# Optimization experiments

Measured on AMD Instinct MI355X. Metric: run time of the kernel, lower is better.

## Reference

```python
import jax, jax.numpy as jnp
import numpy as np

T, D, M1, M2, K = 8192, 512, 2048, 2048, 1024


def setup_inputs() -> dict:
    key = jax.random.key(0)
    k = jax.random.split(key, 6)
    s1 = 1.0 / np.sqrt(D + M1)   # layer 1 init scale (1/sqrt(M1_in + M2_out))
    s2 = 1.0 / np.sqrt(M1 + M2)  # layer 2 init scale
    return {
        "X": jax.random.normal(k[0], (T, D), jnp.float32),
        # RNN layer 1 (D -> M1)
        "Wx1": jax.random.normal(k[1], (D, M1), jnp.float32) * s1,
        "Wh1": jax.random.normal(k[2], (M1, M1), jnp.float32) * s1,
        "bh1": jnp.zeros((M1,), jnp.float32),
        "h01": jnp.zeros((M1,), jnp.float32),
        # RNN layer 2 (M1 -> M2)
        "Wx2": jax.random.normal(k[3], (M1, M2), jnp.float32) * s2,
        "Wh2": jax.random.normal(k[4], (M2, M2), jnp.float32) * s2,
        "bh2": jnp.zeros((M2,), jnp.float32),
        "h02": jnp.zeros((M2,), jnp.float32),
        # logistic = nn.Linear(M2, K); store weight as (M2, K) so y = h @ Wl + bl
        "Wl": jax.random.normal(k[5], (M2, K), jnp.float32) / np.sqrt(M2),
        "bl": jnp.zeros((K,), jnp.float32),
    }


def rnn_layer(X, Wx, Wh, bh, h0):
    # X: (T, Din) -> out: (T, Dout). hidden_t = relu((X@Wx)_t + hidden_{t-1} @ Wh + bh)
    Xp = X @ Wx  # (T, Dout) dense GEMM, precomputed as in the torch code

    def step(h, x):
        h = jax.nn.relu(x + h @ Wh + bh)
        return h, h

    _, out = jax.lax.scan(step, h0, Xp)
    return out


def reference(X, Wx1, Wh1, bh1, h01, Wx2, Wh2, bh2, h02, Wl, bl):
    h = rnn_layer(X, Wx1, Wh1, bh1, h01)
    h = rnn_layer(h, Wx2, Wh2, bh2, h02)
    return h @ Wl + bl  # (T, K) logits
```

## Files before the change

kernel.cpp:

```cpp
#include <hip/hip_runtime.h>
#include <cstdint>
#include <cstddef>

#define TT 8192
#define DD 512
#define MM 2048
#define KK 1024

typedef float f32x4 __attribute__((ext_vector_type(4)));
typedef int   i32x4 __attribute__((ext_vector_type(4)));
typedef unsigned int uint32;

__device__ __forceinline__ void coh_load32(const uint32* p, i32x4& a, i32x4& b) {
  asm volatile("global_load_dwordx4 %0, %2, off sc0 sc1\n\t"
               "global_load_dwordx4 %1, %2, off offset:16 sc0 sc1\n\t"
               "s_waitcnt vmcnt(0)"
               : "=v"(a), "=v"(b) : "v"(p) : "memory");
}
__device__ __forceinline__ void coh_store32(uint32* p, i32x4 a, i32x4 b) {
  asm volatile("global_store_dwordx4 %0, %1, off sc0 sc1\n\t"
               "global_store_dwordx4 %0, %2, off offset:16 sc0 sc1"
               :: "v"(p), "v"(a), "v"(b) : "memory");
}

__device__ __forceinline__ float scrub(float v) {
  return __int_as_float(__float_as_int(v) & 0x7fffffff);
}
__device__ __forceinline__ uint32 bf16r(float f) {
  uint32 u = __float_as_uint(f);
  return (u + 0x7fffu + ((u >> 16) & 1u)) >> 16;
}
__device__ __forceinline__ uint32 pack2(float lo, float hi) {
  return bf16r(lo) | (bf16r(hi) << 16);
}
__device__ __forceinline__ float bflo(uint32 u) { return __uint_as_float(u << 16); }
__device__ __forceinline__ float bfhi(uint32 u) { return __uint_as_float(u & 0xffff0000u); }

__global__ void __launch_bounds__(256) gemm_bias_f32(
    const float* __restrict__ A, const float* __restrict__ B,
    const float* __restrict__ bias, float* __restrict__ C,
    int M, int N, int K)
{
  __shared__ float As[16][128];
  __shared__ float Bs[16][128];
  const int tid = threadIdx.x;
  const int tx = tid & 15, ty = tid >> 4;
  const int row0 = blockIdx.y * 128, col0 = blockIdx.x * 128;
  const int arow = tid >> 1;
  const int ak0  = (tid & 1) * 8;
  const int brow = tid >> 4;
  const int bcol = (tid & 15) * 8;

  const float* Aptr = A + (size_t)(row0 + arow) * K + ak0;
  const float* Bptr = B + (size_t)brow * N + col0 + bcol;

  float acc[8][8];
  #pragma unroll
  for (int i = 0; i < 8; ++i)
    #pragma unroll
    for (int j = 0; j < 8; ++j) acc[i][j] = 0.f;

  for (int kk = 0; kk < K; kk += 16) {
    float4 a0 = *(const float4*)(Aptr + kk);
    float4 a1 = *(const float4*)(Aptr + kk + 4);
    float4 b0 = *(const float4*)(Bptr + (size_t)kk * N);
    float4 b1 = *(const float4*)(Bptr + (size_t)kk * N + 4);
    __syncthreads();
    As[ak0+0][arow] = a0.x; As[ak0+1][arow] = a0.y;
    As[ak0+2][arow] = a0.z; As[ak0+3][arow] = a0.w;
    As[ak0+4][arow] = a1.x; As[ak0+5][arow] = a1.y;
    As[ak0+6][arow] = a1.z; As[ak0+7][arow] = a1.w;
    *(float4*)&Bs[brow][bcol]     = b0;
    *(float4*)&Bs[brow][bcol + 4] = b1;
    __syncthreads();
    #pragma unroll
    for (int k = 0; k < 16; ++k) {
      float4 av0 = *(float4*)&As[k][ty*8];
      float4 av1 = *(float4*)&As[k][ty*8 + 4];
      float4 bv0 = *(float4*)&Bs[k][tx*4];
      float4 bv1 = *(float4*)&Bs[k][64 + tx*4];
      float ar[8] = {av0.x,av0.y,av0.z,av0.w,av1.x,av1.y,av1.z,av1.w};
      float br[8] = {bv0.x,bv0.y,bv0.z,bv0.w,bv1.x,bv1.y,bv1.z,bv1.w};
      #pragma unroll
      for (int i = 0; i < 8; ++i)
        #pragma unroll
        for (int j = 0; j < 8; ++j)
          acc[i][j] += ar[i] * br[j];
    }
  }

  float4 bi0 = *(const float4*)&bias[col0 + tx*4];
  float4 bi1 = *(const float4*)&bias[col0 + 64 + tx*4];
  #pragma unroll
  for (int i = 0; i < 8; ++i) {
    size_t r = (size_t)(row0 + ty*8 + i) * N;
    float4 o0 = make_float4(acc[i][0]+bi0.x, acc[i][1]+bi0.y, acc[i][2]+bi0.z, acc[i][3]+bi0.w);
    float4 o1 = make_float4(acc[i][4]+bi1.x, acc[i][5]+bi1.y, acc[i][6]+bi1.z, acc[i][7]+bi1.w);
    *(float4*)&C[r + col0 + tx*4]      = o0;
    *(float4*)&C[r + col0 + 64 + tx*4] = o1;
  }
}

__global__ void __launch_bounds__(256, 1) rnn_fused(
    const float* __restrict__ Xp1, uint32* __restrict__ H1b,
    uint32* __restrict__ H2b, float* __restrict__ H2f,
    const float* __restrict__ Wh1, const float* __restrict__ Wx2,
    const float* __restrict__ Wh2, const float* __restrict__ h01,
    const float* __restrict__ h02, const float* __restrict__ bh2)
{
  __shared__ __align__(16) unsigned char smem[139392];
  const int tid  = threadIdx.x;
  const int lane = tid & 63;
  const int wv   = tid >> 6;

  if (blockIdx.x < 128) {
    const int w = blockIdx.x;
    float*  WL   = (float*)smem;
    uint32* h1p  = (uint32*)(smem + 131072);
    float*  hout = (float*)(smem + 135168);

    for (int r = 0; r < 8; ++r) {
      const int k = tid + 256*r;
      const float* src = &Wh1[(size_t)k*MM + 16*w];
      #pragma unroll
      for (int c4 = 0; c4 < 4; ++c4) {
        float4 q = *(const float4*)(src + 4*c4);
        WL[(4*c4+0)*2048 + k] = q.x;
        WL[(4*c4+1)*2048 + k] = q.y;
        WL[(4*c4+2)*2048 + k] = q.z;
        WL[(4*c4+3)*2048 + k] = q.w;
      }
    }
    const int cbase = 16*w + 4*wv;
    f32x4 xc = {0.f,0.f,0.f,0.f}, xn = xc;
    if (lane == 0) xc = *(const f32x4*)&Xp1[cbase];
    __syncthreads();

    for (int t = 0; t < TT; ++t) {
      if (tid < 128) {
        const int g = tid;
        if (t == 0) {
          uint32 d[8];
          #pragma unroll
          for (int j = 0; j < 8; ++j)
            d[j] = pack2(h01[16*g + 2*j], h01[16*g + 2*j + 1]);
          *(i32x4*)&h1p[8*g]     = *(i32x4*)&d[0];
          *(i32x4*)&h1p[8*g + 4] = *(i32x4*)&d[4];
        } else {
          const uint32* src = H1b + (size_t)(t-1)*1024 + 8*g;
          i32x4 a, b;
          for (;;) {
            coh_load32(src, a, b);
            if ((((a.x|a.y|a.z|a.w|b.x|b.y|b.z|b.w) & 0x80008000u)) == 0) break;
            __builtin_amdgcn_s_sleep(1);
          }
          *(i32x4*)&h1p[8*g]     = a;
          *(i32x4*)&h1p[8*g + 4] = b;
        }
      }
      if (lane == 0 && t + 1 < TT)
        xn = *(const f32x4*)&Xp1[(size_t)(t+1)*MM + cbase];
      __syncthreads();

      float s0=0.f, s1=0.f, s2=0.f, s3=0.f;
      #pragma unroll
      for (int i = 0; i < 8; ++i) {
        const int k0 = 4*lane + 256*i;
        uint2 dw = *(uint2*)&h1p[k0 >> 1];
        f32x4 h = {bflo(dw.x), bfhi(dw.x), bflo(dw.y), bfhi(dw.y)};
        f32x4 q0 = *(f32x4*)&WL[(4*wv+0)*2048 + k0];
        f32x4 q1 = *(f32x4*)&WL[(4*wv+1)*2048 + k0];
        f32x4 q2 = *(f32x4*)&WL[(4*wv+2)*2048 + k0];
        f32x4 q3 = *(f32x4*)&WL[(4*wv+3)*2048 + k0];
        s0 += h.x*q0.x + h.y*q0.y + h.z*q0.z + h.w*q0.w;
        s1 += h.x*q1.x + h.y*q1.y + h.z*q1.z + h.w*q1.w;
        s2 += h.x*q2.x + h.y*q2.y + h.z*q2.z + h.w*q2.w;
        s3 += h.x*q3.x + h.y*q3.y + h.z*q3.z + h.w*q3.w;
      }
      #pragma unroll
      for (int off = 32; off; off >>= 1) {
        s0 += __shfl_xor(s0, off); s1 += __shfl_xor(s1, off);
        s2 += __shfl_xor(s2, off); s3 += __shfl_xor(s3, off);
      }
      if (lane == 0) {
        f32x4 y;
        y.x = scrub(fmaxf(xc.x + s0, 0.f));
        y.y = scrub(fmaxf(xc.y + s1, 0.f));
        y.z = scrub(fmaxf(xc.z + s2, 0.f));
        y.w = scrub(fmaxf(xc.w + s3, 0.f));
        *(f32x4*)&hout[4*wv] = y;
        xc = xn;
      }
      __syncthreads();

      if (tid == 0) {
        uint32 d[8];
        #pragma unroll
        for (int j = 0; j < 8; ++j) d[j] = pack2(hout[2*j], hout[2*j+1]);
        coh_store32(H1b + (size_t)t*1024 + 8*w, *(i32x4*)&d[0], *(i32x4*)&d[4]);
      }
    }
  } else {
    const int w = blockIdx.x - 128;
    unsigned short* W2p = (unsigned short*)smem;
    uint32* h1p  = (uint32*)(smem + 131072);
    uint32* h2p  = (uint32*)(smem + 135168);
    float*  hout = (float*)(smem + 139264);

    for (int r = 0; r < 16; ++r) {
      const int k = tid + 256*r;
      const float* src = (k < MM) ? &Wx2[(size_t)k*MM + 16*w]
                                  : &Wh2[(size_t)(k-MM)*MM + 16*w];
      #pragma unroll
      for (int c4 = 0; c4 < 4; ++c4) {
        float4 q = *(const float4*)(src + 4*c4);
        const int c = 4*c4;
        W2p[((c+0)>>1)*8192 + 2*k + ((c+0)&1)] = (unsigned short)bf16r(q.x);
        W2p[((c+1)>>1)*8192 + 2*k + ((c+1)&1)] = (unsigned short)bf16r(q.y);
        W2p[((c+2)>>1)*8192 + 2*k + ((c+2)&1)] = (unsigned short)bf16r(q.z);
        W2p[((c+3)>>1)*8192 + 2*k + ((c+3)&1)] = (unsigned short)bf16r(q.w);
      }
    }
    const int cbase = 16*w + 4*wv;
    f32x4 bv = {0.f,0.f,0.f,0.f};
    if (lane == 0) bv = *(const f32x4*)&bh2[cbase];
    __syncthreads();

    const int cp0 = 2*wv;

    for (int t = 0; t < TT; ++t) {
      if (tid < 128) {
        const int g = tid;
        const uint32* p1 = H1b + (size_t)t*1024 + 8*g;
        i32x4 a, b;
        for (;;) {
          coh_load32(p1, a, b);
          if ((((a.x|a.y|a.z|a.w|b.x|b.y|b.z|b.w) & 0x80008000u)) == 0) break;
          __builtin_amdgcn_s_sleep(1);
        }
        *(i32x4*)&h1p[8*g]     = a;
        *(i32x4*)&h1p[8*g + 4] = b;
      }
      __syncthreads();

      float s0=0.f, s1=0.f, s2=0.f, s3=0.f;
      #pragma unroll
      for (int i = 0; i < 8; ++i) {
        const int k0 = 4*lane + 256*i;
        uint2 dw = *(uint2*)&h1p[k0 >> 1];
        f32x4 h = {bflo(dw.x), bfhi(dw.x), bflo(dw.y), bfhi(dw.y)};
        uint4 qa = *(uint4*)&W2p[(cp0+0)*8192 + 2*k0];
        uint4 qb = *(uint4*)&W2p[(cp0+1)*8192 + 2*k0];
        s0 += h.x*bflo(qa.x) + h.y*bflo(qa.y) + h.z*bflo(qa.z) + h.w*bflo(qa.w);
        s1 += h.x*bfhi(qa.x) + h.y*bfhi(qa.y) + h.z*bfhi(qa.z) + h.w*bfhi(qa.w);
        s2 += h.x*bflo(qb.x) + h.y*bflo(qb.y) + h.z*bflo(qb.z) + h.w*bflo(qb.w);
        s3 += h.x*bfhi(qb.x) + h.y*bfhi(qb.y) + h.z*bfhi(qb.z) + h.w*bfhi(qb.w);
      }

      if (tid < 128) {
        const int g = tid;
        if (t == 0) {
          uint32 d[8];
          #pragma unroll
          for (int j = 0; j < 8; ++j)
            d[j] = pack2(h02[16*g + 2*j], h02[16*g + 2*j + 1]);
          *(i32x4*)&h2p[8*g]     = *(i32x4*)&d[0];
          *(i32x4*)&h2p[8*g + 4] = *(i32x4*)&d[4];
        } else {
          const uint32* p2 = H2b + (size_t)(t-1)*1024 + 8*g;
          i32x4 c, d;
          for (;;) {
            coh_load32(p2, c, d);
            if ((((c.x|c.y|c.z|c.w|d.x|d.y|d.z|d.w) & 0x80008000u)) == 0) break;
            __builtin_amdgcn_s_sleep(1);
          }
          *(i32x4*)&h2p[8*g]     = c;
          *(i32x4*)&h2p[8*g + 4] = d;
        }
      }
      __syncthreads();

      #pragma unroll
      for (int i = 0; i < 8; ++i) {
        const int k0 = 4*lane + 256*i;
        const int kw = 2048 + k0;
        uint2 dw = *(uint2*)&h2p[k0 >> 1];
        f32x4 h = {bflo(dw.x), bfhi(dw.x), bflo(dw.y), bfhi(dw.y)};
        uint4 qa = *(uint4*)&W2p[(cp0+0)*8192 + 2*kw];
        uint4 qb = *(uint4*)&W2p[(cp0+1)*8192 + 2*kw];
        s0 += h.x*bflo(qa.x) + h.y*bflo(qa.y) + h.z*bflo(qa.z) + h.w*bflo(qa.w);
        s1 += h.x*bfhi(qa.x) + h.y*bfhi(qa.y) + h.z*bfhi(qa.z) + h.w*bfhi(qa.w);
        s2 += h.x*bflo(qb.x) + h.y*bflo(qb.y) + h.z*bflo(qb.z) + h.w*bflo(qb.w);
        s3 += h.x*bfhi(qb.x) + h.y*bfhi(qb.y) + h.z*bfhi(qb.z) + h.w*bfhi(qb.w);
      }
      #pragma unroll
      for (int off = 32; off; off >>= 1) {
        s0 += __shfl_xor(s0, off); s1 += __shfl_xor(s1, off);
        s2 += __shfl_xor(s2, off); s3 += __shfl_xor(s3, off);
      }
      if (lane == 0) {
        f32x4 y;
        y.x = scrub(fmaxf(s0 + bv.x, 0.f));
        y.y = scrub(fmaxf(s1 + bv.y, 0.f));
        y.z = scrub(fmaxf(s2 + bv.z, 0.f));
        y.w = scrub(fmaxf(s3 + bv.w, 0.f));
        *(f32x4*)&H2f[(size_t)t*MM + cbase] = y;
        *(f32x4*)&hout[4*wv] = y;
      }
      __syncthreads();

      if (tid == 0) {
        uint32 d[8];
        #pragma unroll
        for (int j = 0; j < 8; ++j) d[j] = pack2(hout[2*j], hout[2*j+1]);
        coh_store32(H2b + (size_t)t*1024 + 8*w, *(i32x4*)&d[0], *(i32x4*)&d[4]);
      }
    }
  }
}

__device__ __forceinline__ void coh_load2f(const int* p, i32x4& a, i32x4& b) {
  asm volatile("global_load_dwordx4 %0, %2, off sc0 sc1\n\t"
               "global_load_dwordx4 %1, %2, off offset:16 sc0 sc1\n\t"
               "s_waitcnt vmcnt(0)"
               : "=v"(a), "=v"(b) : "v"(p) : "memory");
}
__global__ void __launch_bounds__(256, 1) rnn_scan_f32(
    const float* __restrict__ Xp, float* __restrict__ H,
    const float* __restrict__ Wh, const float* __restrict__ h0)
{
  __shared__ float h_s[MM];
  __shared__ float h_out[8];
  const int tid  = threadIdx.x;
  const int wg   = blockIdx.x;
  const int lane = tid & 63;
  const int wv   = tid >> 6;
  const int c0   = wg * 8 + wv * 2;

  float4 w0[8], w1[8];
  #pragma unroll
  for (int i = 0; i < 8; ++i) {
    const int kb = lane*4 + 256*i;
    float2 e0 = *(const float2*)&Wh[(size_t)(kb+0)*MM + c0];
    float2 e1 = *(const float2*)&Wh[(size_t)(kb+1)*MM + c0];
    float2 e2 = *(const float2*)&Wh[(size_t)(kb+2)*MM + c0];
    float2 e3 = *(const float2*)&Wh[(size_t)(kb+3)*MM + c0];
    w0[i] = make_float4(e0.x, e1.x, e2.x, e3.x);
    w1[i] = make_float4(e0.y, e1.y, e2.y, e3.y);
  }

  for (int t = 0; t < TT; ++t) {
    float4 ha, hb;
    if (t == 0) {
      ha = ((const float4*)h0)[tid*2];
      hb = ((const float4*)h0)[tid*2 + 1];
    } else {
      const int* src = (const int*)(H + (size_t)(t-1)*MM + tid*8);
      i32x4 a, b;
      do { coh_load2f(src, a, b); }
      while ((a.x | a.y | a.z | a.w | b.x | b.y | b.z | b.w) < 0);
      ha = make_float4(__int_as_float(a.x), __int_as_float(a.y),
                       __int_as_float(a.z), __int_as_float(a.w));
      hb = make_float4(__int_as_float(b.x), __int_as_float(b.y),
                       __int_as_float(b.z), __int_as_float(b.w));
    }
    float xv = 0.f;
    if (lane < 2) xv = Xp[(size_t)t*MM + c0 + lane];
    ((float4*)h_s)[tid*2]     = ha;
    ((float4*)h_s)[tid*2 + 1] = hb;
    __syncthreads();

    float s0 = 0.f, s1 = 0.f;
    #pragma unroll
    for (int i = 0; i < 8; ++i) {
      float4 h4 = *(float4*)&h_s[lane*4 + 256*i];
      s0 += h4.x*w0[i].x + h4.y*w0[i].y + h4.z*w0[i].z + h4.w*w0[i].w;
      s1 += h4.x*w1[i].x + h4.y*w1[i].y + h4.z*w1[i].z + h4.w*w1[i].w;
    }
    #pragma unroll
    for (int off = 32; off; off >>= 1) {
      s0 += __shfl_xor(s0, off);
      s1 += __shfl_xor(s1, off);
    }
    if (lane < 2) {
      float s = (lane == 0) ? s0 : s1;
      h_out[wv*2 + lane] = scrub(fmaxf(xv + s, 0.f));
    }
    __syncthreads();
    if (tid == 0) {
      i32x4 o0 = *(i32x4*)&h_out[0];
      i32x4 o1 = *(i32x4*)&h_out[4];
      coh_store32((uint32*)(H + (size_t)t*MM + wg*8), o0, o1);
    }
  }
}

extern "C" void kernel_launch(void* const* d_in, const int* in_sizes, int n_in,
                              void* d_out, int out_size, void* d_ws, size_t ws_size,
                              hipStream_t stream) {
  (void)in_sizes; (void)n_in; (void)out_size;

  const float* X   = (const float*)d_in[0];
  const float* Wx1 = (const float*)d_in[1];
  const float* Wh1 = (const float*)d_in[2];
  const float* bh1 = (const float*)d_in[3];
  const float* h01 = (const float*)d_in[4];
  const float* Wx2 = (const float*)d_in[5];
  const float* Wh2 = (const float*)d_in[6];
  const float* bh2 = (const float*)d_in[7];
  const float* h02 = (const float*)d_in[8];
  const float* Wl  = (const float*)d_in[9];
  const float* bl  = (const float*)d_in[10];
  float* out = (float*)d_out;

  const size_t NBUF = (size_t)TT * MM;
  dim3 blk(256);

  if (ws_size >= 3 * NBUF * sizeof(float)) {
    float*  Xp1 = (float*)d_ws;
    float*  H2f = Xp1 + NBUF;
    uint32* H1b = (uint32*)(H2f + NBUF);
    uint32* H2b = H1b + (size_t)TT * 1024;

    (void)hipMemsetAsync(H1b, 0xFF, 2 * (size_t)TT * 1024 * sizeof(uint32), stream);

    gemm_bias_f32<<<dim3(MM/128, TT/128), blk, 0, stream>>>(X, Wx1, bh1, Xp1, TT, MM, DD);

    {
      const float* xp = Xp1; uint32* h1b = H1b; uint32* h2b = H2b; float* h2f = H2f;
      const float* wh1 = Wh1; const float* wx2 = Wx2; const float* wh2 = Wh2;
      const float* h01p = h01; const float* h02p = h02; const float* bh2p = bh2;
      void* args[] = {&xp, &h1b, &h2b, &h2f, &wh1, &wx2, &wh2, &h01p, &h02p, &bh2p};
      (void)hipLaunchCooperativeKernel((const void*)rnn_fused, dim3(256), blk, args, 0, stream);
    }

    gemm_bias_f32<<<dim3(KK/128, TT/128), blk, 0, stream>>>(H2f, Wl, bl, out, TT, KK, MM);
  } else {
    float* bufA = (float*)d_ws;
    float* bufB = bufA + NBUF;

    (void)hipMemsetAsync(bufB, 0xFF, NBUF * sizeof(float), stream);
    gemm_bias_f32<<<dim3(MM/128, TT/128), blk, 0, stream>>>(X, Wx1, bh1, bufA, TT, MM, DD);
    {
      const float* xp = bufA; float* h = bufB; const float* wh = Wh1; const float* h0p = h01;
      void* args[] = {&xp, &h, &wh, &h0p};
      (void)hipLaunchCooperativeKernel((const void*)rnn_scan_f32, dim3(256), blk, args, 0, stream);
    }
    gemm_bias_f32<<<dim3(MM/128, TT/128), blk, 0, stream>>>(bufB, Wx2, bh2, bufA, TT, MM, MM);
    (void)hipMemsetAsync(bufB, 0xFF, NBUF * sizeof(float), stream);
    {
      const float* xp = bufA; float* h = bufB; const float* wh = Wh2; const float* h0p = h02;
      void* args[] = {&xp, &h, &wh, &h0p};
      (void)hipLaunchCooperativeKernel((const void*)rnn_scan_f32, dim3(256), blk, args, 0, stream);
    }
    gemm_bias_f32<<<dim3(KK/128, TT/128), blk, 0, stream>>>(bufA, Wl, bl, out, TT, KK, MM);
  }
}
```

Before: 24.13 ms.

## Prefetch next H1 and overlap H2 polling with compute in fused RNN

Each wave's lane 0 now writes its packed bf16 outputs straight to the global exchange buffer, which removes a barrier and the single-thread gather/store step per timestep. The layer-2 blocks double-buffer the layer-1 hidden state in LDS. They issue non-blocking loads for the next H1 row and the previous H2 row before the matvec, then wait only afterwards, so global-memory latency overlaps the compute. The layer-1 spin loop drops its sleep. The cost is more complex synchronization and a risk of subtle ordering bugs across blocks.

Result: slower. 29.89 ms (+23.9%).

```diff
diff --git a/kernel.cpp b/kernel.cpp
--- a/kernel.cpp
+++ b/kernel.cpp
@@ -9,6 +9,7 @@
 
 typedef float f32x4 __attribute__((ext_vector_type(4)));
 typedef int   i32x4 __attribute__((ext_vector_type(4)));
+typedef int   i32x2 __attribute__((ext_vector_type(2)));
 typedef unsigned int uint32;
 
 __device__ __forceinline__ void coh_load32(const uint32* p, i32x4& a, i32x4& b) {
@@ -17,12 +18,23 @@
                "s_waitcnt vmcnt(0)"
                : "=v"(a), "=v"(b) : "v"(p) : "memory");
 }
+__device__ __forceinline__ void issue32(const uint32* p, i32x4& a, i32x4& b) {
+  asm volatile("global_load_dwordx4 %0, %2, off sc0 sc1\n\t"
+               "global_load_dwordx4 %1, %2, off offset:16 sc0 sc1"
+               : "=v"(a), "=v"(b) : "v"(p) : "memory");
+}
+__device__ __forceinline__ void coh_store8(uint32* p, i32x2 v) {
+  asm volatile("global_store_dwordx2 %0, %1, off sc0 sc1" :: "v"(p), "v"(v) : "memory");
+}
 __device__ __forceinline__ void coh_store32(uint32* p, i32x4 a, i32x4 b) {
   asm volatile("global_store_dwordx4 %0, %1, off sc0 sc1\n\t"
                "global_store_dwordx4 %0, %2, off offset:16 sc0 sc1"
                :: "v"(p), "v"(a), "v"(b) : "memory");
 }
 
+__device__ __forceinline__ int sent8(i32x4 a, i32x4 b) {
+  return ((a.x|a.y|a.z|a.w|b.x|b.y|b.z|b.w) & 0x80008000u) != 0;
+}
 __device__ __forceinline__ float scrub(float v) {
   return __int_as_float(__float_as_int(v) & 0x7fffffff);
 }
@@ -108,16 +120,15 @@
     const float* __restrict__ Wh2, const float* __restrict__ h01,
     const float* __restrict__ h02, const float* __restrict__ bh2)
 {
-  __shared__ __align__(16) unsigned char smem[139392];
+  __shared__ __align__(16) unsigned char smem[143360];
   const int tid  = threadIdx.x;
   const int lane = tid & 63;
   const int wv   = tid >> 6;
 
   if (blockIdx.x < 128) {
     const int w = blockIdx.x;
-    float*  WL   = (float*)smem;
-    uint32* h1p  = (uint32*)(smem + 131072);
-    float*  hout = (float*)(smem + 135168);
+    float*  WL  = (float*)smem;
+    uint32* h1p = (uint32*)(smem + 131072);
 
     for (int r = 0; r < 8; ++r) {
       const int k = tid + 256*r;
@@ -138,24 +149,19 @@
 
     for (int t = 0; t < TT; ++t) {
       if (tid < 128) {
-        const int g = tid;
         if (t == 0) {
           uint32 d[8];
           #pragma unroll
           for (int j = 0; j < 8; ++j)
-            d[j] = pack2(h01[16*g + 2*j], h01[16*g + 2*j + 1]);
-          *(i32x4*)&h1p[8*g]     = *(i32x4*)&d[0];
-          *(i32x4*)&h1p[8*g + 4] = *(i32x4*)&d[4];
+            d[j] = pack2(h01[16*tid + 2*j], h01[16*tid + 2*j + 1]);
+          *(i32x4*)&h1p[8*tid]     = *(i32x4*)&d[0];
+          *(i32x4*)&h1p[8*tid + 4] = *(i32x4*)&d[4];
         } else {
-          const uint32* src = H1b + (size_t)(t-1)*1024 + 8*g;
+          const uint32* src = H1b + (size_t)(t-1)*1024 + 8*tid;
           i32x4 a, b;
-          for (;;) {
-            coh_load32(src, a, b);
-            if ((((a.x|a.y|a.z|a.w|b.x|b.y|b.z|b.w) & 0x80008000u)) == 0) break;
-            __builtin_amdgcn_s_sleep(1);
-          }
-          *(i32x4*)&h1p[8*g]     = a;
-          *(i32x4*)&h1p[8*g + 4] = b;
+          do { coh_load32(src, a, b); } while (sent8(a, b));
+          *(i32x4*)&h1p[8*tid]     = a;
+          *(i32x4*)&h1p[8*tid + 4] = b;
         }
       }
       if (lane == 0 && t + 1 < TT)
@@ -183,29 +189,22 @@
         s2 += __shfl_xor(s2, off); s3 += __shfl_xor(s3, off);
       }
       if (lane == 0) {
-        f32x4 y;
-        y.x = scrub(fmaxf(xc.x + s0, 0.f));
-        y.y = scrub(fmaxf(xc.y + s1, 0.f));
-        y.z = scrub(fmaxf(xc.z + s2, 0.f));
-        y.w = scrub(fmaxf(xc.w + s3, 0.f));
-        *(f32x4*)&hout[4*wv] = y;
+        float y0 = scrub(fmaxf(xc.x + s0, 0.f));
+        float y1 = scrub(fmaxf(xc.y + s1, 0.f));
+        float y2 = scrub(fmaxf(xc.z + s2, 0.f));
+        float y3 = scrub(fmaxf(xc.w + s3, 0.f));
+        i32x2 d; d.x = (int)pack2(y0, y1); d.y = (int)pack2(y2, y3);
+        coh_store8(H1b + (size_t)t*1024 + 8*w + 2*wv, d);
         xc = xn;
       }
       __syncthreads();
-
-      if (tid == 0) {
-        uint32 d[8];
-        #pragma unroll
-        for (int j = 0; j < 8; ++j) d[j] = pack2(hout[2*j], hout[2*j+1]);
-        coh_store32(H1b + (size_t)t*1024 + 8*w, *(i32x4*)&d[0], *(i32x4*)&d[4]);
-      }
     }
   } else {
     const int w = blockIdx.x - 128;
-    unsigned short* W2p = (unsigned short*)smem;
-    uint32* h1p  = (uint32*)(smem + 131072);
-    uint32* h2p  = (uint32*)(smem + 135168);
-    float*  hout = (float*)(smem + 139264);
+    unsigned short* W2p  = (unsigned short*)smem;
+    uint32* h1buf0 = (uint32*)(smem + 131072);
+    uint32* h1buf1 = (uint32*)(smem + 135168);
+    uint32* h2p    = (uint32*)(smem + 139264);
 
     for (int r = 0; r < 16; ++r) {
       const int k = tid + 256*r;
@@ -226,28 +225,36 @@
     if (lane == 0) bv = *(const f32x4*)&bh2[cbase];
     __syncthreads();
 
+    if (tid < 128) {
+      const uint32* p1 = H1b + 8*tid;
+      i32x4 a, b;
+      for (;;) {
+        coh_load32(p1, a, b);
+        if (!sent8(a, b)) break;
+        __builtin_amdgcn_s_sleep(1);
+      }
+      *(i32x4*)&h1buf0[8*tid]     = a;
+      *(i32x4*)&h1buf0[8*tid + 4] = b;
+    }
+    __syncthreads();
+
     const int cp0 = 2*wv;
 
     for (int t = 0; t < TT; ++t) {
+      uint32* bufc = (t & 1) ? h1buf1 : h1buf0;
+      uint32* bufn = (t & 1) ? h1buf0 : h1buf1;
+
+      i32x4 sa = {0,0,0,0}, sb = sa, pa = sa, pb = sa;
       if (tid < 128) {
-        const int g = tid;
-        const uint32* p1 = H1b + (size_t)t*1024 + 8*g;
-        i32x4 a, b;
-        for (;;) {
-          coh_load32(p1, a, b);
-          if ((((a.x|a.y|a.z|a.w|b.x|b.y|b.z|b.w) & 0x80008000u)) == 0) break;
-          __builtin_amdgcn_s_sleep(1);
-        }
-        *(i32x4*)&h1p[8*g]     = a;
-        *(i32x4*)&h1p[8*g + 4] = b;
-      }
-      __syncthreads();
+        if (t > 0)      issue32(H2b + (size_t)(t-1)*1024 + 8*tid, sa, sb);
+        if (t + 1 < TT) issue32(H1b + (size_t)(t+1)*1024 + 8*tid, pa, pb);
+      }
 
       float s0=0.f, s1=0.f, s2=0.f, s3=0.f;
       #pragma unroll
       for (int i = 0; i < 8; ++i) {
         const int k0 = 4*lane + 256*i;
-        uint2 dw = *(uint2*)&h1p[k0 >> 1];
+        uint2 dw = *(uint2*)&bufc[k0 >> 1];
         f32x4 h = {bflo(dw.x), bfhi(dw.x), bflo(dw.y), bfhi(dw.y)};
         uint4 qa = *(uint4*)&W2p[(cp0+0)*8192 + 2*k0];
         uint4 qb = *(uint4*)&W2p[(cp0+1)*8192 + 2*k0];
@@ -258,24 +265,23 @@
       }
 
       if (tid < 128) {
-        const int g = tid;
+        asm volatile("s_waitcnt vmcnt(0)"
+                     : "+v"(sa), "+v"(sb), "+v"(pa), "+v"(pb) :: "memory");
+        __builtin_amdgcn_sched_barrier(0);
         if (t == 0) {
           uint32 d[8];
           #pragma unroll
           for (int j = 0; j < 8; ++j)
-            d[j] = pack2(h02[16*g + 2*j], h02[16*g + 2*j + 1]);
-          *(i32x4*)&h2p[8*g]     = *(i32x4*)&d[0];
-          *(i32x4*)&h2p[8*g + 4] = *(i32x4*)&d[4];
+            d[j] = pack2(h02[16*tid + 2*j], h02[16*tid + 2*j + 1]);
+          *(i32x4*)&h2p[8*tid]     = *(i32x4*)&d[0];
+          *(i32x4*)&h2p[8*tid + 4] = *(i32x4*)&d[4];
         } else {
-          const uint32* p2 = H2b + (size_t)(t-1)*1024 + 8*g;
-          i32x4 c, d;
-          for (;;) {
-            coh_load32(p2, c, d);
-            if ((((c.x|c.y|c.z|c.w|d.x|d.y|d.z|d.w) & 0x80008000u)) == 0) break;
-            __builtin_amdgcn_s_sleep(1);
+          if (sent8(sa, sb)) {
+            const uint32* p2 = H2b + (size_t)(t-1)*1024 + 8*tid;
+            do { coh_load32(p2, sa, sb); } while (sent8(sa, sb));
           }
-          *(i32x4*)&h2p[8*g]     = c;
-          *(i32x4*)&h2p[8*g + 4] = d;
+          *(i32x4*)&h2p[8*tid]     = sa;
+          *(i32x4*)&h2p[8*tid + 4] = sb;
         }
       }
       __syncthreads();
@@ -299,32 +305,33 @@
         s2 += __shfl_xor(s2, off); s3 += __shfl_xor(s3, off);
       }
       if (lane == 0) {
-        f32x4 y;
-        y.x = scrub(fmaxf(s0 + bv.x, 0.f));
-        y.y = scrub(fmaxf(s1 + bv.y, 0.f));
-        y.z = scrub(fmaxf(s2 + bv.z, 0.f));
-        y.w = scrub(fmaxf(s3 + bv.w, 0.f));
+        float y0 = scrub(fmaxf(s0 + bv.x, 0.f));
+        float y1 = scrub(fmaxf(s1 + bv.y, 0.f));
+        float y2 = scrub(fmaxf(s2 + bv.z, 0.f));
+        float y3 = scrub(fmaxf(s3 + bv.w, 0.f));
+        i32x2 d; d.x = (int)pack2(y0, y1); d.y = (int)pack2(y2, y3);
+        coh_store8(H2b + (size_t)t*1024 + 8*w + 2*wv, d);
+        f32x4 y = {y0, y1, y2, y3};
         *(f32x4*)&H2f[(size_t)t*MM + cbase] = y;
-        *(f32x4*)&hout[4*wv] = y;
+      }
+
+      if (tid < 128 && t + 1 < TT) {
+        if (sent8(pa, pb)) {
+          const uint32* p1 = H1b + (size_t)(t+1)*1024 + 8*tid;
+          for (;;) {
+            coh_load32(p1, pa, pb);
+            if (!sent8(pa, pb)) break;
+            __builtin_amdgcn_s_sleep(1);
+          }
+        }
+        *(i32x4*)&bufn[8*tid]     = pa;
+        *(i32x4*)&bufn[8*tid + 4] = pb;
       }
       __syncthreads();
-
-      if (tid == 0) {
-        uint32 d[8];
-        #pragma unroll
-        for (int j = 0; j < 8; ++j) d[j] = pack2(hout[2*j], hout[2*j+1]);
-        coh_store32(H2b + (size_t)t*1024 + 8*w, *(i32x4*)&d[0], *(i32x4*)&d[4]);
-      }
-    }
-  }
-}
-
-__device__ __forceinline__ void coh_load2f(const int* p, i32x4& a, i32x4& b) {
-  asm volatile("global_load_dwordx4 %0, %2, off sc0 sc1\n\t"
-               "global_load_dwordx4 %1, %2, off offset:16 sc0 sc1\n\t"
-               "s_waitcnt vmcnt(0)"
-               : "=v"(a), "=v"(b) : "v"(p) : "memory");
-}
+    }
+  }
+}
+
 __global__ void __launch_bounds__(256, 1) rnn_scan_f32(
     const float* __restrict__ Xp, float* __restrict__ H,
     const float* __restrict__ Wh, const float* __restrict__ h0)
@@ -355,9 +362,9 @@
       ha = ((const float4*)h0)[tid*2];
       hb = ((const float4*)h0)[tid*2 + 1];
     } else {
-      const int* src = (const int*)(H + (size_t)(t-1)*MM + tid*8);
+      const uint32* src = (const uint32*)(H + (size_t)(t-1)*MM + tid*8);
       i32x4 a, b;
-      do { coh_load2f(src, a, b); }
+      do { coh_load32(src, a, b); }
       while ((a.x | a.y | a.z | a.w | b.x | b.y | b.z | b.w) < 0);
       ha = make_float4(__int_as_float(a.x), __int_as_float(a.y),
                        __int_as_float(a.z), __int_as_float(a.w));
```

## Double-buffer layer-1 hidden state in layer-2 blocks and drop polling sleep

Applied to the files above, without the earlier changes.

Layer-2 blocks now keep two shared buffers for the incoming layer-1 hidden vector. The poll for step t+1 is issued at the end of step t, after the H2 store, so the separate wait and barrier at the top of each step go away and the fetch is off the start of the Wx2 dot product. The layer-1 poll loop also drops its s_sleep so it spins without backoff, which may react faster but puts more traffic on memory. Shared memory grows by one 4 KB buffer, and a duplicate coherent-load helper is removed.

Result: no change. 24.60 ms (+2.0%).

```diff
diff --git a/kernel.cpp b/kernel.cpp
--- a/kernel.cpp
+++ b/kernel.cpp
@@ -23,6 +23,9 @@
                :: "v"(p), "v"(a), "v"(b) : "memory");
 }
 
+__device__ __forceinline__ int sent8(i32x4 a, i32x4 b) {
+  return ((a.x|a.y|a.z|a.w|b.x|b.y|b.z|b.w) & 0x80008000u) != 0;
+}
 __device__ __forceinline__ float scrub(float v) {
   return __int_as_float(__float_as_int(v) & 0x7fffffff);
 }
@@ -108,7 +111,7 @@
     const float* __restrict__ Wh2, const float* __restrict__ h01,
     const float* __restrict__ h02, const float* __restrict__ bh2)
 {
-  __shared__ __align__(16) unsigned char smem[139392];
+  __shared__ __align__(16) unsigned char smem[143424];
   const int tid  = threadIdx.x;
   const int lane = tid & 63;
   const int wv   = tid >> 6;
@@ -138,24 +141,19 @@
 
     for (int t = 0; t < TT; ++t) {
       if (tid < 128) {
-        const int g = tid;
         if (t == 0) {
           uint32 d[8];
           #pragma unroll
           for (int j = 0; j < 8; ++j)
-            d[j] = pack2(h01[16*g + 2*j], h01[16*g + 2*j + 1]);
-          *(i32x4*)&h1p[8*g]     = *(i32x4*)&d[0];
-          *(i32x4*)&h1p[8*g + 4] = *(i32x4*)&d[4];
+            d[j] = pack2(h01[16*tid + 2*j], h01[16*tid + 2*j + 1]);
+          *(i32x4*)&h1p[8*tid]     = *(i32x4*)&d[0];
+          *(i32x4*)&h1p[8*tid + 4] = *(i32x4*)&d[4];
         } else {
-          const uint32* src = H1b + (size_t)(t-1)*1024 + 8*g;
+          const uint32* src = H1b + (size_t)(t-1)*1024 + 8*tid;
           i32x4 a, b;
-          for (;;) {
-            coh_load32(src, a, b);
-            if ((((a.x|a.y|a.z|a.w|b.x|b.y|b.z|b.w) & 0x80008000u)) == 0) break;
-            __builtin_amdgcn_s_sleep(1);
-          }
-          *(i32x4*)&h1p[8*g]     = a;
-          *(i32x4*)&h1p[8*g + 4] = b;
+          do { coh_load32(src, a, b); } while (sent8(a, b));
+          *(i32x4*)&h1p[8*tid]     = a;
+          *(i32x4*)&h1p[8*tid + 4] = b;
         }
       }
       if (lane == 0 && t + 1 < TT)
@@ -202,10 +200,11 @@
     }
   } else {
     const int w = blockIdx.x - 128;
-    unsigned short* W2p = (unsigned short*)smem;
-    uint32* h1p  = (uint32*)(smem + 131072);
-    uint32* h2p  = (uint32*)(smem + 135168);
-    float*  hout = (float*)(smem + 139264);
+    unsigned short* W2p  = (unsigned short*)smem;
+    uint32* h1buf0 = (uint32*)(smem + 131072);
+    uint32* h1buf1 = (uint32*)(smem + 135168);
+    uint32* h2p    = (uint32*)(smem + 139264);
+    float*  hout   = (float*)(smem + 143360);
 
     for (int r = 0; r < 16; ++r) {
       const int k = tid + 256*r;
@@ -226,28 +225,30 @@
     if (lane == 0) bv = *(const f32x4*)&bh2[cbase];
     __syncthreads();
 
+    if (tid < 128) {
+      const uint32* p1 = H1b + 8*tid;
+      i32x4 a, b;
+      for (;;) {
+        coh_load32(p1, a, b);
+        if (!sent8(a, b)) break;
+        __builtin_amdgcn_s_sleep(1);
+      }
+      *(i32x4*)&h1buf0[8*tid]     = a;
+      *(i32x4*)&h1buf0[8*tid + 4] = b;
+    }
+    __syncthreads();
+
     const int cp0 = 2*wv;
 
     for (int t = 0; t < TT; ++t) {
-      if (tid < 128) {
-        const int g = tid;
-        const uint32* p1 = H1b + (size_t)t*1024 + 8*g;
-        i32x4 a, b;
-        for (;;) {
-          coh_load32(p1, a, b);
-          if ((((a.x|a.y|a.z|a.w|b.x|b.y|b.z|b.w) & 0x80008000u)) == 0) break;
-          __builtin_amdgcn_s_sleep(1);
-        }
-        *(i32x4*)&h1p[8*g]     = a;
-        *(i32x4*)&h1p[8*g + 4] = b;
-      }
-      __syncthreads();
+      uint32* bufc = (t & 1) ? h1buf1 : h1buf0;
+      uint32* bufn = (t & 1) ? h1buf0 : h1buf1;
 
       float s0=0.f, s1=0.f, s2=0.f, s3=0.f;
       #pragma unroll
       for (int i = 0; i < 8; ++i) {
         const int k0 = 4*lane + 256*i;
-        uint2 dw = *(uint2*)&h1p[k0 >> 1];
+        uint2 dw = *(uint2*)&bufc[k0 >> 1];
         f32x4 h = {bflo(dw.x), bfhi(dw.x), bflo(dw.y), bfhi(dw.y)};
         uint4 qa = *(uint4*)&W2p[(cp0+0)*8192 + 2*k0];
         uint4 qb = *(uint4*)&W2p[(cp0+1)*8192 + 2*k0];
@@ -258,24 +259,23 @@
       }
 
       if (tid < 128) {
-        const int g = tid;
         if (t == 0) {
           uint32 d[8];
           #pragma unroll
           for (int j = 0; j < 8; ++j)
-            d[j] = pack2(h02[16*g + 2*j], h02[16*g + 2*j + 1]);
-          *(i32x4*)&h2p[8*g]     = *(i32x4*)&d[0];
-          *(i32x4*)&h2p[8*g + 4] = *(i32x4*)&d[4];
+            d[j] = pack2(h02[16*tid + 2*j], h02[16*tid + 2*j + 1]);
+          *(i32x4*)&h2p[8*tid]     = *(i32x4*)&d[0];
+          *(i32x4*)&h2p[8*tid + 4] = *(i32x4*)&d[4];
         } else {
-          const uint32* p2 = H2b + (size_t)(t-1)*1024 + 8*g;
+          const uint32* p2 = H2b + (size_t)(t-1)*1024 + 8*tid;
           i32x4 c, d;
           for (;;) {
             coh_load32(p2, c, d);
-            if ((((c.x|c.y|c.z|c.w|d.x|d.y|d.z|d.w) & 0x80008000u)) == 0) break;
+            if (!sent8(c, d)) break;
             __builtin_amdgcn_s_sleep(1);
           }
-          *(i32x4*)&h2p[8*g]     = c;
-          *(i32x4*)&h2p[8*g + 4] = d;
+          *(i32x4*)&h2p[8*tid]     = c;
+          *(i32x4*)&h2p[8*tid + 4] = d;
         }
       }
       __syncthreads();
@@ -315,16 +315,23 @@
         for (int j = 0; j < 8; ++j) d[j] = pack2(hout[2*j], hout[2*j+1]);
         coh_store32(H2b + (size_t)t*1024 + 8*w, *(i32x4*)&d[0], *(i32x4*)&d[4]);
       }
-    }
-  }
-}
-
-__device__ __forceinline__ void coh_load2f(const int* p, i32x4& a, i32x4& b) {
-  asm volatile("global_load_dwordx4 %0, %2, off sc0 sc1\n\t"
-               "global_load_dwordx4 %1, %2, off offset:16 sc0 sc1\n\t"
-               "s_waitcnt vmcnt(0)"
-               : "=v"(a), "=v"(b) : "v"(p) : "memory");
-}
+
+      if (tid < 128 && t + 1 < TT) {
+        const uint32* p1 = H1b + (size_t)(t+1)*1024 + 8*tid;
+        i32x4 a, b;
+        for (;;) {
+          coh_load32(p1, a, b);
+          if (!sent8(a, b)) break;
+          __builtin_amdgcn_s_sleep(1);
+        }
+        *(i32x4*)&bufn[8*tid]     = a;
+        *(i32x4*)&bufn[8*tid + 4] = b;
+      }
+      __syncthreads();
+    }
+  }
+}
+
 __global__ void __launch_bounds__(256, 1) rnn_scan_f32(
     const float* __restrict__ Xp, float* __restrict__ H,
     const float* __restrict__ Wh, const float* __restrict__ h0)
@@ -355,9 +362,9 @@
       ha = ((const float4*)h0)[tid*2];
       hb = ((const float4*)h0)[tid*2 + 1];
     } else {
-      const int* src = (const int*)(H + (size_t)(t-1)*MM + tid*8);
+      const uint32* src = (const uint32*)(H + (size_t)(t-1)*MM + tid*8);
       i32x4 a, b;
-      do { coh_load2f(src, a, b); }
+      do { coh_load32(src, a, b); }
       while ((a.x | a.y | a.z | a.w | b.x | b.y | b.z | b.w) < 0);
       ha = make_float4(__int_as_float(a.x), __int_as_float(a.y),
                        __int_as_float(a.z), __int_as_float(a.w));
```
